# Optimization experiments

Measured on AMD Instinct MI355X. Metric: run time of the kernel, lower is better.

Reference implementation:

```python
import jax, jax.numpy as jnp
import numpy as np

N, D_IN, D_HID, D_BOX = 4096, 512, 256, 22
W_SCALE = 0.02  # keep exp(WA) numerically tame


def setup_inputs() -> dict:
    key = jax.random.key(0)
    ks = jax.random.split(key, 10)
    inp = {
        'input_x': jax.random.normal(ks[0], (N, D_IN), dtype=jnp.float32),
        'box': jax.random.normal(ks[1], (N, D_BOX), dtype=jnp.float32),
        # Linear weights stored as [in, out] so y = x @ W
        'WG1': jax.random.normal(ks[2], (D_BOX, D_HID), dtype=jnp.float32) * W_SCALE,
        'WK1': jax.random.normal(ks[3], (D_IN, D_HID), dtype=jnp.float32) * W_SCALE,
        'WQ1': jax.random.normal(ks[4], (D_IN, D_HID), dtype=jnp.float32) * W_SCALE,
        'WV1': jax.random.normal(ks[5], (D_IN, D_HID), dtype=jnp.float32) * W_SCALE,
        'WG2': jax.random.normal(ks[6], (D_BOX, D_HID), dtype=jnp.float32) * W_SCALE,
        'WK2': jax.random.normal(ks[7], (D_IN, D_HID), dtype=jnp.float32) * W_SCALE,
        'WQ2': jax.random.normal(ks[8], (D_IN, D_HID), dtype=jnp.float32) * W_SCALE,
        'WV2': jax.random.normal(ks[9], (D_IN, D_HID), dtype=jnp.float32) * W_SCALE,
    }
    return inp


def _branch(x, box, WG, WK, WQ, WV):
    K = x @ WK                      # [N, 256]
    Q = x @ WQ                      # [N, 256]
    WA = (K @ Q.T) / 16.0           # [N, N]
    G = box @ WG                    # [N, 256]
    WGm = jax.nn.relu((G @ G.T) / 16.0)  # [N, N]
    S = WGm * jnp.exp(WA)           # relu-gated exponential scores
    W = S / jnp.sum(S)              # GLOBAL (whole-matrix) normalization
    return W @ (x @ WV)             # [N, 256]


def reference(input_x, box, WG1, WK1, WQ1, WV1, WG2, WK2, WQ2, WV2):
    FR1 = _branch(input_x, box, WG1, WK1, WQ1, WV1)
    FR2 = _branch(input_x, box, WG2, WK2, WQ2, WV2)
    FR = jnp.concatenate((FR1, FR2), axis=1)  # [N, 512]
    return FR * 0.1 + input_x
```

## Files before the change

kernel.cpp:

```cpp
#include <hip/hip_runtime.h>
#include <hip/hip_bf16.h>
#include <hip/hip_fp16.h>

using bf16 = __hip_bfloat16;
typedef __attribute__((ext_vector_type(8))) short short8;
typedef __attribute__((ext_vector_type(4))) float f32x4;

#define NROW 4096
#define DIN  512
#define DH   256
#define DBOX 22
#define BK   32
#define BKU  64
#define KSPL 8

#define NORM_LO 118
#define NORM_HI 130
#define WT_LO   110
#define WT_HI   126

static __device__ __forceinline__ f32x4 mfma16(short8 a, short8 b, f32x4 c) {
  return __builtin_amdgcn_mfma_f32_16x16x32_bf16(a, b, c, 0, 0, 0);
}
static __device__ __forceinline__ short8 ldg8(const bf16* p) {
  return *reinterpret_cast<const short8*>(p);
}

static __device__ int detect_mode(const void* src, int lo, int hi) {
  __shared__ int cLo, cHi;
  if (threadIdx.x == 0) { cLo = 0; cHi = 0; }
  __syncthreads();
  const unsigned* w = (const unsigned*)src;
  int l = 0, h = 0;
  for (int t = threadIdx.x; t < 1024; t += 256) {
    unsigned v = w[t];
    int elo = (int)((v >> 7) & 0xFF);
    int ehi = (int)((v >> 23) & 0xFF);
    l += (elo >= lo && elo <= hi) ? 1 : 0;
    h += (ehi >= lo && ehi <= hi) ? 1 : 0;
  }
#pragma unroll
  for (int off = 32; off > 0; off >>= 1) {
    l += __shfl_down(l, off, 64);
    h += __shfl_down(h, off, 64);
  }
  if ((threadIdx.x & 63) == 0) { atomicAdd(&cLo, l); atomicAdd(&cHi, h); }
  __syncthreads();
  int lowCnt = cLo, hiCnt = cHi;
  __syncthreads();
  if (lowCnt > 700) return 1;
  if (hiCnt  > 700) return 0;
  return 2;
}

static __device__ __forceinline__ float load_as_float(const void* src, long i, int mode) {
  if (mode == 1) return __bfloat162float(((const bf16*)src)[i]);
  if (mode == 0) return ((const float*)src)[i];
  return __half2float(((const __half*)src)[i]);
}

static __device__ __forceinline__ void store_as(void* dst, long i, float v, int mode) {
  if (mode == 1)      ((bf16*)dst)[i]   = __float2bfloat16(v);
  else if (mode == 2) ((__half*)dst)[i] = __float2half(v);
  else                ((float*)dst)[i]  = v;
}

struct ConvArgs { const void* src[4]; bf16* dst[4]; };

__global__ __launch_bounds__(256) void convert_kernel(ConvArgs a) {
  int b = blockIdx.x, seg, base;
  if (b < 8192)      { seg = 0; base = b; }
  else if (b < 8544) { seg = 1; base = b - 8192; }
  else if (b < 8566) { seg = 2; base = b - 8544; }
  else               { seg = 3; base = b - 8566; }
  int lo = (seg < 2) ? NORM_LO : WT_LO;
  int hi = (seg < 2) ? NORM_HI : WT_HI;
  int mode = detect_mode(a.src[seg], lo, hi);
  int i = base * 256 + threadIdx.x;
  a.dst[seg][i] = __float2bfloat16(load_as_float(a.src[seg], i, mode));
}

struct WTArgs { const void* src[6]; bf16* dst[6]; };

__global__ __launch_bounds__(256) void wtrans_kernel(WTArgs a) {
  const int which = blockIdx.z;
  int mode = detect_mode(a.src[which], WT_LO, WT_HI);
  __shared__ float tile[64][65];
  const int tr = blockIdx.x * 64;
  const int tc = blockIdx.y * 64;
  const int rin = threadIdx.x >> 6;
  const int cin = threadIdx.x & 63;
#pragma unroll
  for (int p = 0; p < 16; ++p) {
    int r = rin + p * 4;
    tile[r][cin] = load_as_float(a.src[which], (long)(tr + r) * DH + tc + cin, mode);
  }
  __syncthreads();
#pragma unroll
  for (int p = 0; p < 16; ++p) {
    int r = rin + p * 4;
    a.dst[which][(long)(tc + r) * DIN + tr + cin] = __float2bfloat16(tile[cin][r]);
  }
}

struct ProjArgs { const bf16* Wcat[2]; bf16* CK[2]; bf16* CQ[2]; bf16* VT[2]; };

__global__ __launch_bounds__(256, 3) void proj_kernel(const bf16* __restrict__ X, ProjArgs a) {
  const int z = blockIdx.z;
  const bf16* __restrict__ W = a.Wcat[z];
  __shared__ __align__(16) bf16 Xa[128 * BKU], Wb[128 * BKU];
  const int tid = threadIdx.x;
  const int wave = tid >> 6, lane = tid & 63;
  const int quad = lane >> 4, l16 = lane & 15;
  const int i0 = blockIdx.x * 128, n0 = blockIdx.y * 128;
  const int rw = (wave & 1) * 64, cw = (wave >> 1) * 64;

  int soff[4], grow[4], gko[4];
#pragma unroll
  for (int c = 0; c < 4; ++c) {
    int m = c * 256 + tid;
    int row = m >> 3, chunk = m & 7;
    grow[c] = row; gko[c] = chunk * 8;
    soff[c] = row * BKU + ((chunk ^ (row & 7)) * 8);
  }

  short8 pf[8];
  auto load_tiles = [&](int k0) {
#pragma unroll
    for (int c = 0; c < 4; ++c) {
      pf[c]     = ldg8(X + (long)(i0 + grow[c]) * DIN + k0 + gko[c]);
      pf[c + 4] = ldg8(W + (long)(n0 + grow[c]) * DIN + k0 + gko[c]);
    }
  };

  f32x4 acc[4][4];
#pragma unroll
  for (int p = 0; p < 4; ++p)
#pragma unroll
    for (int q = 0; q < 4; ++q) acc[p][q] = (f32x4){0,0,0,0};

  load_tiles(0);
  for (int kt = 0; kt < DIN / BKU; ++kt) {
    __syncthreads();
#pragma unroll
    for (int c = 0; c < 4; ++c) {
      *(short8*)&Xa[soff[c]] = pf[c];
      *(short8*)&Wb[soff[c]] = pf[c + 4];
    }
    __syncthreads();
    if (kt + 1 < DIN / BKU) load_tiles((kt + 1) * BKU);

#pragma unroll
    for (int kk = 0; kk < 2; ++kk) {
      short8 ax[4];
#pragma unroll
      for (int ti = 0; ti < 4; ++ti) {
        int row = rw + ti * 16 + l16;
        ax[ti] = *(const short8*)&Xa[row * BKU + (((kk * 4 + quad) ^ (row & 7)) * 8)];
      }
#pragma unroll
      for (int tj = 0; tj < 4; ++tj) {
        int row = cw + tj * 16 + l16;
        short8 bw = *(const short8*)&Wb[row * BKU + (((kk * 4 + quad) ^ (row & 7)) * 8)];
#pragma unroll
        for (int ti = 0; ti < 4; ++ti) acc[ti][tj] = mfma16(ax[ti], bw, acc[ti][tj]);
      }
    }
  }

#pragma unroll
  for (int ti = 0; ti < 4; ++ti) {
#pragma unroll
    for (int tj = 0; tj < 4; ++tj) {
#pragma unroll
      for (int r = 0; r < 4; ++r) {
        int row = i0 + rw + ti * 16 + quad * 4 + r;
        int n = n0 + cw + tj * 16 + l16;
        bf16 v = __float2bfloat16(acc[ti][tj][r]);
        if (n < 256)      a.CK[z][(long)row * DH + n] = v;
        else if (n < 512) a.CQ[z][(long)row * DH + n - 256] = v;
        else              a.VT[z][(long)(n - 512) * NROW + row] = v;
      }
    }
  }
}

struct M22Args { const bf16* WG[2]; float* M[2]; };

__global__ __launch_bounds__(256) void m22_kernel(M22Args a) {
  const int z = blockIdx.x;
  const bf16* WG = a.WG[z];
  for (int p = threadIdx.x; p < DBOX * DBOX; p += 256) {
    int r = p / DBOX, c = p % DBOX;
    float acc = 0.f;
    for (int k = 0; k < DH; ++k)
      acc += __bfloat162float(WG[r * DH + k]) * __bfloat162float(WG[c * DH + k]);
    a.M[z][p] = acc;
  }
}

struct PPArgs { const float* M[2]; const bf16* Boxb; bf16* P[2]; bf16* Boxp; };

__global__ __launch_bounds__(256) void p_prep_kernel(PPArgs a) {
  const int z = blockIdx.y;
  __shared__ float Ml[DBOX * DBOX];
  for (int t = threadIdx.x; t < DBOX * DBOX; t += 256) Ml[t] = a.M[z][t];
  __syncthreads();
  int idx = blockIdx.x * 256 + threadIdx.x;
  int r = idx >> 5, c = idx & 31;
  float val = 0.f;
  if (c < DBOX) {
#pragma unroll
    for (int k = 0; k < DBOX; ++k)
      val += __bfloat162float(a.Boxb[r * DBOX + k]) * Ml[k * DBOX + c];
  }
  a.P[z][idx] = __float2bfloat16(val);
  if (z == 0)
    a.Boxp[idx] = (c < DBOX) ? a.Boxb[r * DBOX + c] : __float2bfloat16(0.f);
}

struct ScoreArgs { const bf16 *K[2], *Q[2], *P[2]; const bf16* B; bf16* S[2]; float* sum; };

__global__ __launch_bounds__(256, 2) void score_kernel(ScoreArgs a) {
  const int z = blockIdx.z;
  const bf16* __restrict__ K = a.K[z];
  const bf16* __restrict__ Q = a.Q[z];
  __shared__ __align__(16) bf16 Kt[128 * BK], Qt[128 * BK], Pi[128 * BK], Bj[128 * BK];
  const int tid = threadIdx.x;
  const int wave = tid >> 6, lane = tid & 63;
  const int quad = lane >> 4, l16 = lane & 15;
  const int i0 = blockIdx.x * 128, j0 = blockIdx.y * 128;
  const int rw = (wave & 1) * 64, cw = (wave >> 1) * 64;

  int soff[2], grow[2], gko[2];
#pragma unroll
  for (int c = 0; c < 2; ++c) {
    int m = c * 256 + tid;
    int row = m >> 2, chunk = m & 3;
    grow[c] = row; gko[c] = chunk * 8;
    soff[c] = row * BK + ((chunk ^ (row & 3)) * 8);
  }

#pragma unroll
  for (int c = 0; c < 2; ++c) {
    *(short8*)&Pi[soff[c]] = ldg8(a.P[z] + (long)(i0 + grow[c]) * 32 + gko[c]);
    *(short8*)&Bj[soff[c]] = ldg8(a.B + (long)(j0 + grow[c]) * 32 + gko[c]);
  }

  short8 pf[4];
  auto load_tiles = [&](int k0) {
#pragma unroll
    for (int c = 0; c < 2; ++c) {
      pf[c * 2 + 0] = ldg8(K + (long)(i0 + grow[c]) * DH + k0 + gko[c]);
      pf[c * 2 + 1] = ldg8(Q + (long)(j0 + grow[c]) * DH + k0 + gko[c]);
    }
  };

  f32x4 wa[4][4];
#pragma unroll
  for (int p = 0; p < 4; ++p)
#pragma unroll
    for (int q = 0; q < 4; ++q) wa[p][q] = (f32x4){0,0,0,0};

  load_tiles(0);
  for (int kt = 0; kt < DH / BK; ++kt) {
    __syncthreads();
#pragma unroll
    for (int c = 0; c < 2; ++c) {
      *(short8*)&Kt[soff[c]] = pf[c * 2 + 0];
      *(short8*)&Qt[soff[c]] = pf[c * 2 + 1];
    }
    __syncthreads();
    if (kt + 1 < DH / BK) load_tiles((kt + 1) * BK);

    short8 aK[4];
#pragma unroll
    for (int ti = 0; ti < 4; ++ti) {
      int row = rw + ti * 16 + l16;
      aK[ti] = *(const short8*)&Kt[row * BK + ((quad ^ (row & 3)) * 8)];
    }
#pragma unroll
    for (int tj = 0; tj < 4; ++tj) {
      int row = cw + tj * 16 + l16;
      short8 bQ = *(const short8*)&Qt[row * BK + ((quad ^ (row & 3)) * 8)];
#pragma unroll
      for (int ti = 0; ti < 4; ++ti) wa[ti][tj] = mfma16(aK[ti], bQ, wa[ti][tj]);
    }
  }

  f32x4 gm[4][4];
  {
    short8 aP[4];
#pragma unroll
    for (int ti = 0; ti < 4; ++ti) {
      int row = rw + ti * 16 + l16;
      aP[ti] = *(const short8*)&Pi[row * BK + ((quad ^ (row & 3)) * 8)];
    }
#pragma unroll
    for (int tj = 0; tj < 4; ++tj) {
      int row = cw + tj * 16 + l16;
      short8 bB = *(const short8*)&Bj[row * BK + ((quad ^ (row & 3)) * 8)];
#pragma unroll
      for (int ti = 0; ti < 4; ++ti)
        gm[ti][tj] = mfma16(aP[ti], bB, (f32x4){0.f, 0.f, 0.f, 0.f});
    }
  }

  float lsum = 0.f;
  bf16* __restrict__ S = a.S[z];
#pragma unroll
  for (int ti = 0; ti < 4; ++ti) {
#pragma unroll
    for (int tj = 0; tj < 4; ++tj) {
#pragma unroll
      for (int r = 0; r < 4; ++r) {
        float g = gm[ti][tj][r] * 0.0625f;
        g = (g > 0.f) ? g : 0.f;
        float s = g * __expf(fminf(wa[ti][tj][r] * 0.0625f, 30.f));
        s = fminf(s, 1e30f);
        lsum += s;
        S[(long)(i0 + rw + ti * 16 + quad * 4 + r) * NROW + j0 + cw + tj * 16 + l16] =
            __float2bfloat16(s);
      }
    }
  }

  __shared__ float wsum[4];
#pragma unroll
  for (int off = 32; off > 0; off >>= 1) lsum += __shfl_down(lsum, off, 64);
  if (lane == 0) wsum[wave] = lsum;
  __syncthreads();
  if (tid == 0) atomicAdd(a.sum + z, wsum[0] + wsum[1] + wsum[2] + wsum[3]);
}

struct UVArgs { const bf16 *S[2], *VT[2]; float* Up; };

__global__ __launch_bounds__(256, 3) void uv_kernel(UVArgs a) {
  const int z = blockIdx.y >> 1;
  const int nh = blockIdx.y & 1;
  const int ks = blockIdx.z;
  const bf16* __restrict__ S = a.S[z];
  const bf16* __restrict__ VT = a.VT[z];
  float* __restrict__ U = a.Up + ((size_t)(z * KSPL + ks)) * NROW * DH;
  __shared__ __align__(16) bf16 St[128 * BKU], Vt[128 * BKU];
  const int tid = threadIdx.x;
  const int wave = tid >> 6, lane = tid & 63;
  const int quad = lane >> 4, l16 = lane & 15;
  const int i0 = blockIdx.x * 128;
  const int n0 = nh * 128;
  const int kbase = ks * (NROW / KSPL);
  const int rw = (wave & 1) * 64, cw = (wave >> 1) * 64;

  int soff[4], grow[4], gko[4];
#pragma unroll
  for (int c = 0; c < 4; ++c) {
    int m = c * 256 + tid;
    int row = m >> 3, chunk = m & 7;
    grow[c] = row; gko[c] = chunk * 8;
    soff[c] = row * BKU + ((chunk ^ (row & 7)) * 8);
  }

  short8 pf[8];
  auto load_tiles = [&](int k0) {
#pragma unroll
    for (int c = 0; c < 4; ++c) {
      pf[c]     = ldg8(S + (long)(i0 + grow[c]) * NROW + k0 + gko[c]);
      pf[c + 4] = ldg8(VT + (long)(n0 + grow[c]) * NROW + k0 + gko[c]);
    }
  };

  f32x4 acc[4][4];
#pragma unroll
  for (int p = 0; p < 4; ++p)
#pragma unroll
    for (int q = 0; q < 4; ++q) acc[p][q] = (f32x4){0,0,0,0};

  load_tiles(kbase);
  for (int kt = 0; kt < (NROW / KSPL) / BKU; ++kt) {
    __syncthreads();
#pragma unroll
    for (int c = 0; c < 4; ++c) {
      *(short8*)&St[soff[c]] = pf[c];
      *(short8*)&Vt[soff[c]] = pf[c + 4];
    }
    __syncthreads();
    if (kt + 1 < (NROW / KSPL) / BKU) load_tiles(kbase + (kt + 1) * BKU);

#pragma unroll
    for (int kk = 0; kk < 2; ++kk) {
      short8 aS[4];
#pragma unroll
      for (int ti = 0; ti < 4; ++ti) {
        int row = rw + ti * 16 + l16;
        aS[ti] = *(const short8*)&St[row * BKU + (((kk * 4 + quad) ^ (row & 7)) * 8)];
      }
#pragma unroll
      for (int tj = 0; tj < 4; ++tj) {
        int row = cw + tj * 16 + l16;
        short8 bV = *(const short8*)&Vt[row * BKU + (((kk * 4 + quad) ^ (row & 7)) * 8)];
#pragma unroll
        for (int ti = 0; ti < 4; ++ti) acc[ti][tj] = mfma16(aS[ti], bV, acc[ti][tj]);
      }
    }
  }

#pragma unroll
  for (int ti = 0; ti < 4; ++ti)
#pragma unroll
    for (int tj = 0; tj < 4; ++tj)
#pragma unroll
      for (int r = 0; r < 4; ++r)
        U[(long)(i0 + rw + ti * 16 + quad * 4 + r) * DH + n0 + cw + tj * 16 + l16] =
            acc[ti][tj][r];
}

__global__ __launch_bounds__(256) void epilogue_kernel(
    const void* __restrict__ xraw, const float* __restrict__ Up,
    const float* __restrict__ sums, void* __restrict__ out) {
  int mode = detect_mode(xraw, NORM_LO, NORM_HI);
  int idx = blockIdx.x * 256 + threadIdx.x;
  int r = idx >> 9, c = idx & 511;
  int z = (c < 256) ? 0 : 1;
  long e = (long)r * DH + (c & 255);
  const float* base = Up + (size_t)z * KSPL * NROW * DH;
  float u = 0.f;
#pragma unroll
  for (int ks = 0; ks < KSPL; ++ks) u += base[(size_t)ks * NROW * DH + e];
  float s = sums[z];
  float fr = u * 0.1f / s;
  fr = (fr == fr) ? fminf(fmaxf(fr, -0.05f), 0.05f) : 0.f;
  float xv = load_as_float(xraw, idx, mode);
  store_as(out, idx, xv + fr, mode);
}

__global__ __launch_bounds__(256) void xcopy_kernel(const void* __restrict__ xraw,
                                                    void* __restrict__ out) {
  int mode = detect_mode(xraw, NORM_LO, NORM_HI);
  int idx = blockIdx.x * 256 + threadIdx.x;
  store_as(out, idx, load_as_float(xraw, idx, mode), mode);
}

extern "C" void kernel_launch(void* const* d_in, const int* in_sizes, int n_in,
                              void* d_out, int out_size, void* d_ws, size_t ws_size,
                              hipStream_t stream) {
  int ix = -1, ib = -1, wgp[2] = {-1, -1}, sixp[6] = {-1,-1,-1,-1,-1,-1};
  int nwg = 0, nsix = 0;
  for (int i = 0; i < n_in; ++i) {
    int s = in_sizes[i];
    if (s == NROW * DIN) ix = i;
    else if (s == NROW * DBOX) ib = i;
    else if (s == DIN * DH && nsix < 6) sixp[nsix++] = i;
    else if (s == DBOX * DH && nwg < 2) wgp[nwg++] = i;
  }

  if (ix < 0 || ib < 0 || nsix != 6 || nwg != 2 || ws_size < 170u * 1024u * 1024u) {
    const void* xsrc = (ix >= 0) ? d_in[ix] : d_in[0];
    xcopy_kernel<<<dim3(NROW * DIN / 256), 256, 0, stream>>>(xsrc, d_out);
    return;
  }

  const void *pK1, *pQ1, *pV1, *pK2, *pQ2, *pV2, *pG1, *pG2;
  if (wgp[0] == 0 && wgp[1] == 1) {
    pK1 = d_in[sixp[0]]; pK2 = d_in[sixp[1]];
    pQ1 = d_in[sixp[2]]; pQ2 = d_in[sixp[3]];
    pV1 = d_in[sixp[4]]; pV2 = d_in[sixp[5]];
    pG1 = d_in[wgp[0]];  pG2 = d_in[wgp[1]];
  } else if (wgp[0] == 3 && wgp[1] == 7) {
    pV2 = d_in[sixp[0]]; pQ2 = d_in[sixp[1]]; pK2 = d_in[sixp[2]];
    pV1 = d_in[sixp[3]]; pQ1 = d_in[sixp[4]]; pK1 = d_in[sixp[5]];
    pG2 = d_in[wgp[0]];  pG1 = d_in[wgp[1]];
  } else {
    pK1 = d_in[sixp[0]]; pQ1 = d_in[sixp[1]]; pV1 = d_in[sixp[2]];
    pK2 = d_in[sixp[3]]; pQ2 = d_in[sixp[4]]; pV2 = d_in[sixp[5]];
    pG1 = d_in[wgp[0]];  pG2 = d_in[wgp[1]];
  }
  const void* input_x = d_in[ix];
  const void* box     = d_in[ib];

  char* ws = (char*)d_ws;
  size_t off = 0;
  auto alloc = [&](size_t bytes) { char* p = ws + off; off += (bytes + 255) & ~size_t(255); return p; };

  const size_t M_BYTES  = (size_t)NROW * DH * 2;

  bf16* Xb    = (bf16*)alloc((size_t)NROW * DIN * 2);
  bf16* Boxb  = (bf16*)alloc((size_t)NROW * DBOX * 2);
  bf16* WG1b  = (bf16*)alloc((size_t)DBOX * DH * 2);
  bf16* WG2b  = (bf16*)alloc((size_t)DBOX * DH * 2);
  bf16* Wcat1 = (bf16*)alloc((size_t)768 * DIN * 2);
  bf16* Wcat2 = (bf16*)alloc((size_t)768 * DIN * 2);
  bf16* K1 = (bf16*)alloc(M_BYTES);
  bf16* Q1 = (bf16*)alloc(M_BYTES);
  bf16* K2 = (bf16*)alloc(M_BYTES);
  bf16* Q2 = (bf16*)alloc(M_BYTES);
  bf16* VT1 = (bf16*)alloc(M_BYTES);
  bf16* VT2 = (bf16*)alloc(M_BYTES);
  float* M1 = (float*)alloc(DBOX * DBOX * 4);
  float* M2 = (float*)alloc(DBOX * DBOX * 4);
  bf16* P1   = (bf16*)alloc((size_t)NROW * 32 * 2);
  bf16* P2   = (bf16*)alloc((size_t)NROW * 32 * 2);
  bf16* Boxp = (bf16*)alloc((size_t)NROW * 32 * 2);
  float* sums = (float*)alloc(256);
  float* Up = (float*)alloc((size_t)2 * KSPL * NROW * DH * 4);
  bf16* S1 = (bf16*)alloc((size_t)NROW * NROW * 2);
  bf16* S2 = (bf16*)alloc((size_t)NROW * NROW * 2);

  (void)hipMemsetAsync(sums, 0, 256, stream);

  ConvArgs ca;
  ca.src[0] = input_x; ca.dst[0] = Xb;
  ca.src[1] = box;     ca.dst[1] = Boxb;
  ca.src[2] = pG1;     ca.dst[2] = WG1b;
  ca.src[3] = pG2;     ca.dst[3] = WG2b;
  convert_kernel<<<dim3(8588), 256, 0, stream>>>(ca);

  WTArgs wa;
  wa.src[0] = pK1; wa.dst[0] = Wcat1;
  wa.src[1] = pQ1; wa.dst[1] = Wcat1 + (size_t)256 * DIN;
  wa.src[2] = pV1; wa.dst[2] = Wcat1 + (size_t)512 * DIN;
  wa.src[3] = pK2; wa.dst[3] = Wcat2;
  wa.src[4] = pQ2; wa.dst[4] = Wcat2 + (size_t)256 * DIN;
  wa.src[5] = pV2; wa.dst[5] = Wcat2 + (size_t)512 * DIN;
  wtrans_kernel<<<dim3(8, 4, 6), 256, 0, stream>>>(wa);

  M22Args ma;
  ma.WG[0] = WG1b; ma.WG[1] = WG2b;
  ma.M[0] = M1;    ma.M[1] = M2;
  m22_kernel<<<dim3(2), 256, 0, stream>>>(ma);

  PPArgs ppa;
  ppa.M[0] = M1; ppa.M[1] = M2;
  ppa.Boxb = Boxb;
  ppa.P[0] = P1; ppa.P[1] = P2;
  ppa.Boxp = Boxp;
  p_prep_kernel<<<dim3(512, 2), 256, 0, stream>>>(ppa);

  ProjArgs pa;
  pa.Wcat[0] = Wcat1; pa.Wcat[1] = Wcat2;
  pa.CK[0] = K1; pa.CQ[0] = Q1; pa.VT[0] = VT1;
  pa.CK[1] = K2; pa.CQ[1] = Q2; pa.VT[1] = VT2;
  proj_kernel<<<dim3(32, 6, 2), 256, 0, stream>>>(Xb, pa);

  ScoreArgs sa;
  sa.K[0] = K1; sa.K[1] = K2;
  sa.Q[0] = Q1; sa.Q[1] = Q2;
  sa.P[0] = P1; sa.P[1] = P2;
  sa.B = Boxp;
  sa.S[0] = S1; sa.S[1] = S2;
  sa.sum = sums;
  score_kernel<<<dim3(32, 32, 2), 256, 0, stream>>>(sa);

  UVArgs ua;
  ua.S[0] = S1;  ua.S[1] = S2;
  ua.VT[0] = VT1; ua.VT[1] = VT2;
  ua.Up = Up;
  uv_kernel<<<dim3(32, 4, KSPL), 256, 0, stream>>>(ua);

  epilogue_kernel<<<dim3(NROW * DIN / 256), 256, 0, stream>>>(input_x, Up, sums, d_out);
}
```

Before: 227.8 us.

## Fuse score and S·V kernels to keep score tiles in shared memory

Replaces the separate score kernel (which wrote two 4096x4096 bf16 score matrices to global memory) and the split-K S·V kernel with a single fused kernel. Each block holds a 64-row K tile in LDS, computes 64x128 score tiles, stores them in a swizzled shared buffer and immediately multiplies by V^T, accumulating into registers. The split count drops from 8 to 4, which shrinks the partial-sum buffer the epilogue reads. This removes roughly 64MB of score write/read traffic, at the cost of reading Q and V^T directly from global memory without LDS staging, smaller per-block tiles, and a grid of 512 blocks.

```diff
diff --git a/kernel.cpp b/kernel.cpp
--- a/kernel.cpp
+++ b/kernel.cpp
@@ -10,9 +10,8 @@
 #define DIN  512
 #define DH   256
 #define DBOX 22
-#define BK   32
 #define BKU  64
-#define KSPL 8
+#define KSPL 4
 
 #define NORM_LO 118
 #define NORM_HI 130
@@ -219,199 +218,175 @@
     a.Boxp[idx] = (c < DBOX) ? a.Boxb[r * DBOX + c] : __float2bfloat16(0.f);
 }
 
-struct ScoreArgs { const bf16 *K[2], *Q[2], *P[2]; const bf16* B; bf16* S[2]; float* sum; };
-
-__global__ __launch_bounds__(256, 2) void score_kernel(ScoreArgs a) {
-  const int z = blockIdx.z;
-  const bf16* __restrict__ K = a.K[z];
-  const bf16* __restrict__ Q = a.Q[z];
-  __shared__ __align__(16) bf16 Kt[128 * BK], Qt[128 * BK], Pi[128 * BK], Bj[128 * BK];
-  const int tid = threadIdx.x;
+struct FuseArgs {
+  const bf16 *K[2], *Q[2], *VT[2], *P[2];
+  const bf16* B;
+  float* Up;
+  float* sum;
+};
+
+__global__ __launch_bounds__(256, 2) void fused_kernel(FuseArgs a) {
+  const int bid = blockIdx.x;
+  const int wl  = (bid & 7) * 64 + (bid >> 3);
+  const int ib  = wl & 63;
+  const int ks  = (wl >> 6) & 3;
+  const int z   = wl >> 8;
+
+  const bf16* __restrict__ K  = a.K[z];
+  const bf16* __restrict__ Q  = a.Q[z];
+  const bf16* __restrict__ VT = a.VT[z];
+  const bf16* __restrict__ P  = a.P[z];
+  const bf16* __restrict__ B  = a.B;
+  float* __restrict__ U = a.Up + ((size_t)(z * KSPL + ks)) * NROW * DH;
+
+  __shared__ __align__(16) bf16 Ksh[64 * DH];
+  __shared__ __align__(16) bf16 Ssh[64 * 128];
+  __shared__ float wsum[4];
+
+  const int tid  = threadIdx.x;
   const int wave = tid >> 6, lane = tid & 63;
   const int quad = lane >> 4, l16 = lane & 15;
-  const int i0 = blockIdx.x * 128, j0 = blockIdx.y * 128;
-  const int rw = (wave & 1) * 64, cw = (wave >> 1) * 64;
-
-  int soff[2], grow[2], gko[2];
-#pragma unroll
-  for (int c = 0; c < 2; ++c) {
+  const int i0    = ib * 64;
+  const int jbase = ks * (NROW / KSPL);
+  const int cw = wave * 32;
+  const int nw = wave * 64;
+
+#pragma unroll
+  for (int c = 0; c < 8; ++c) {
     int m = c * 256 + tid;
-    int row = m >> 2, chunk = m & 3;
-    grow[c] = row; gko[c] = chunk * 8;
-    soff[c] = row * BK + ((chunk ^ (row & 3)) * 8);
-  }
-
-#pragma unroll
-  for (int c = 0; c < 2; ++c) {
-    *(short8*)&Pi[soff[c]] = ldg8(a.P[z] + (long)(i0 + grow[c]) * 32 + gko[c]);
-    *(short8*)&Bj[soff[c]] = ldg8(a.B + (long)(j0 + grow[c]) * 32 + gko[c]);
-  }
-
-  short8 pf[4];
-  auto load_tiles = [&](int k0) {
-#pragma unroll
-    for (int c = 0; c < 2; ++c) {
-      pf[c * 2 + 0] = ldg8(K + (long)(i0 + grow[c]) * DH + k0 + gko[c]);
-      pf[c * 2 + 1] = ldg8(Q + (long)(j0 + grow[c]) * DH + k0 + gko[c]);
+    int row = m >> 5, g = m & 31;
+    short8 v = ldg8(K + (long)(i0 + row) * DH + g * 8);
+    *(short8*)((char*)Ksh + row * 512 + ((g ^ (row & 7)) * 16)) = v;
+  }
+
+  short8 pfr[4];
+#pragma unroll
+  for (int ti = 0; ti < 4; ++ti)
+    pfr[ti] = ldg8(P + (long)(i0 + ti * 16 + l16) * 32 + quad * 8);
+
+  f32x4 acc[4][4];
+#pragma unroll
+  for (int p = 0; p < 4; ++p)
+#pragma unroll
+    for (int q = 0; q < 4; ++q) acc[p][q] = (f32x4){0, 0, 0, 0};
+  float lsum = 0.f;
+
+  __syncthreads();
+
+  for (int jt = 0; jt < (NROW / KSPL) / 128; ++jt) {
+    const int j0 = jbase + jt * 128;
+
+    f32x4 wa[4][2];
+#pragma unroll
+    for (int p = 0; p < 4; ++p) { wa[p][0] = (f32x4){0,0,0,0}; wa[p][1] = (f32x4){0,0,0,0}; }
+
+    short8 bb[2];
+#pragma unroll
+    for (int tj = 0; tj < 2; ++tj)
+      bb[tj] = ldg8(B + (long)(j0 + cw + tj * 16 + l16) * 32 + quad * 8);
+
+    short8 qf[2];
+#pragma unroll
+    for (int tj = 0; tj < 2; ++tj)
+      qf[tj] = ldg8(Q + (long)(j0 + cw + tj * 16 + l16) * DH + quad * 8);
+
+#pragma unroll
+    for (int kt = 0; kt < 8; ++kt) {
+      short8 qn[2];
+      if (kt < 7) {
+#pragma unroll
+        for (int tj = 0; tj < 2; ++tj)
+          qn[tj] = ldg8(Q + (long)(j0 + cw + tj * 16 + l16) * DH + (kt + 1) * 32 + quad * 8);
+      }
+      short8 kf[4];
+#pragma unroll
+      for (int ti = 0; ti < 4; ++ti) {
+        int row = ti * 16 + l16;
+        kf[ti] = *(const short8*)((const char*)Ksh + row * 512 +
+                                  (((kt * 4 + quad) ^ (row & 7)) * 16));
+      }
+#pragma unroll
+      for (int tj = 0; tj < 2; ++tj)
+#pragma unroll
+        for (int ti = 0; ti < 4; ++ti)
+          wa[ti][tj] = mfma16(kf[ti], qf[tj], wa[ti][tj]);
+      if (kt < 7) { qf[0] = qn[0]; qf[1] = qn[1]; }
     }
-  };
-
-  f32x4 wa[4][4];
-#pragma unroll
-  for (int p = 0; p < 4; ++p)
-#pragma unroll
-    for (int q = 0; q < 4; ++q) wa[p][q] = (f32x4){0,0,0,0};
-
-  load_tiles(0);
-  for (int kt = 0; kt < DH / BK; ++kt) {
+
+    f32x4 gm[4][2];
+#pragma unroll
+    for (int tj = 0; tj < 2; ++tj)
+#pragma unroll
+      for (int ti = 0; ti < 4; ++ti)
+        gm[ti][tj] = mfma16(pfr[ti], bb[tj], (f32x4){0.f, 0.f, 0.f, 0.f});
+
     __syncthreads();
-#pragma unroll
-    for (int c = 0; c < 2; ++c) {
-      *(short8*)&Kt[soff[c]] = pf[c * 2 + 0];
-      *(short8*)&Qt[soff[c]] = pf[c * 2 + 1];
+
+#pragma unroll
+    for (int ti = 0; ti < 4; ++ti)
+#pragma unroll
+      for (int tj = 0; tj < 2; ++tj)
+#pragma unroll
+        for (int r = 0; r < 4; ++r) {
+          float g = gm[ti][tj][r] * 0.0625f;
+          g = (g > 0.f) ? g : 0.f;
+          float s = g * __expf(fminf(wa[ti][tj][r] * 0.0625f, 30.f));
+          s = fminf(s, 1e30f);
+          lsum += s;
+          int row = ti * 16 + quad * 4 + r;
+          int col = cw + tj * 16 + l16;
+          *(bf16*)((char*)Ssh + row * 256 + ((col * 2) ^ ((row & 7) << 4))) =
+              __float2bfloat16(s);
+        }
+
+    short8 vf[4];
+#pragma unroll
+    for (int tn = 0; tn < 4; ++tn)
+      vf[tn] = ldg8(VT + (long)(nw + tn * 16 + l16) * NROW + j0 + quad * 8);
+
+    __syncthreads();
+
+#pragma unroll
+    for (int s4 = 0; s4 < 4; ++s4) {
+      short8 vn[4];
+      if (s4 < 3) {
+#pragma unroll
+        for (int tn = 0; tn < 4; ++tn)
+          vn[tn] = ldg8(VT + (long)(nw + tn * 16 + l16) * NROW + j0 + (s4 + 1) * 32 + quad * 8);
+      }
+      short8 sf[4];
+#pragma unroll
+      for (int ti = 0; ti < 4; ++ti) {
+        int row = ti * 16 + l16;
+        sf[ti] = *(const short8*)((const char*)Ssh + row * 256 +
+                                  ((s4 * 64 + quad * 16) ^ ((row & 7) << 4)));
+      }
+#pragma unroll
+      for (int tn = 0; tn < 4; ++tn)
+#pragma unroll
+        for (int ti = 0; ti < 4; ++ti)
+          acc[ti][tn] = mfma16(sf[ti], vf[tn], acc[ti][tn]);
+      if (s4 < 3) {
+#pragma unroll
+        for (int tn = 0; tn < 4; ++tn) vf[tn] = vn[tn];
+      }
     }
-    __syncthreads();
-    if (kt + 1 < DH / BK) load_tiles((kt + 1) * BK);
-
-    short8 aK[4];
-#pragma unroll
-    for (int ti = 0; ti < 4; ++ti) {
-      int row = rw + ti * 16 + l16;
-      aK[ti] = *(const short8*)&Kt[row * BK + ((quad ^ (row & 3)) * 8)];
-    }
-#pragma unroll
-    for (int tj = 0; tj < 4; ++tj) {
-      int row = cw + tj * 16 + l16;
-      short8 bQ = *(const short8*)&Qt[row * BK + ((quad ^ (row & 3)) * 8)];
-#pragma unroll
-      for (int ti = 0; ti < 4; ++ti) wa[ti][tj] = mfma16(aK[ti], bQ, wa[ti][tj]);
-    }
-  }
-
-  f32x4 gm[4][4];
-  {
-    short8 aP[4];
-#pragma unroll
-    for (int ti = 0; ti < 4; ++ti) {
-      int row = rw + ti * 16 + l16;
-      aP[ti] = *(const short8*)&Pi[row * BK + ((quad ^ (row & 3)) * 8)];
-    }
-#pragma unroll
-    for (int tj = 0; tj < 4; ++tj) {
-      int row = cw + tj * 16 + l16;
-      short8 bB = *(const short8*)&Bj[row * BK + ((quad ^ (row & 3)) * 8)];
-#pragma unroll
-      for (int ti = 0; ti < 4; ++ti)
-        gm[ti][tj] = mfma16(aP[ti], bB, (f32x4){0.f, 0.f, 0.f, 0.f});
-    }
-  }
-
-  float lsum = 0.f;
-  bf16* __restrict__ S = a.S[z];
-#pragma unroll
-  for (int ti = 0; ti < 4; ++ti) {
-#pragma unroll
-    for (int tj = 0; tj < 4; ++tj) {
-#pragma unroll
-      for (int r = 0; r < 4; ++r) {
-        float g = gm[ti][tj][r] * 0.0625f;
-        g = (g > 0.f) ? g : 0.f;
-        float s = g * __expf(fminf(wa[ti][tj][r] * 0.0625f, 30.f));
-        s = fminf(s, 1e30f);
-        lsum += s;
-        S[(long)(i0 + rw + ti * 16 + quad * 4 + r) * NROW + j0 + cw + tj * 16 + l16] =
-            __float2bfloat16(s);
-      }
-    }
-  }
-
-  __shared__ float wsum[4];
+  }
+
+#pragma unroll
+  for (int ti = 0; ti < 4; ++ti)
+#pragma unroll
+    for (int tn = 0; tn < 4; ++tn)
+#pragma unroll
+      for (int r = 0; r < 4; ++r)
+        U[(long)(i0 + ti * 16 + quad * 4 + r) * DH + nw + tn * 16 + l16] =
+            acc[ti][tn][r];
+
 #pragma unroll
   for (int off = 32; off > 0; off >>= 1) lsum += __shfl_down(lsum, off, 64);
   if (lane == 0) wsum[wave] = lsum;
   __syncthreads();
   if (tid == 0) atomicAdd(a.sum + z, wsum[0] + wsum[1] + wsum[2] + wsum[3]);
-}
-
-struct UVArgs { const bf16 *S[2], *VT[2]; float* Up; };
-
-__global__ __launch_bounds__(256, 3) void uv_kernel(UVArgs a) {
-  const int z = blockIdx.y >> 1;
-  const int nh = blockIdx.y & 1;
-  const int ks = blockIdx.z;
-  const bf16* __restrict__ S = a.S[z];
-  const bf16* __restrict__ VT = a.VT[z];
-  float* __restrict__ U = a.Up + ((size_t)(z * KSPL + ks)) * NROW * DH;
-  __shared__ __align__(16) bf16 St[128 * BKU], Vt[128 * BKU];
-  const int tid = threadIdx.x;
-  const int wave = tid >> 6, lane = tid & 63;
-  const int quad = lane >> 4, l16 = lane & 15;
-  const int i0 = blockIdx.x * 128;
-  const int n0 = nh * 128;
-  const int kbase = ks * (NROW / KSPL);
-  const int rw = (wave & 1) * 64, cw = (wave >> 1) * 64;
-
-  int soff[4], grow[4], gko[4];
-#pragma unroll
-  for (int c = 0; c < 4; ++c) {
-    int m = c * 256 + tid;
-    int row = m >> 3, chunk = m & 7;
-    grow[c] = row; gko[c] = chunk * 8;
-    soff[c] = row * BKU + ((chunk ^ (row & 7)) * 8);
-  }
-
-  short8 pf[8];
-  auto load_tiles = [&](int k0) {
-#pragma unroll
-    for (int c = 0; c < 4; ++c) {
-      pf[c]     = ldg8(S + (long)(i0 + grow[c]) * NROW + k0 + gko[c]);
-      pf[c + 4] = ldg8(VT + (long)(n0 + grow[c]) * NROW + k0 + gko[c]);
-    }
-  };
-
-  f32x4 acc[4][4];
-#pragma unroll
-  for (int p = 0; p < 4; ++p)
-#pragma unroll
-    for (int q = 0; q < 4; ++q) acc[p][q] = (f32x4){0,0,0,0};
-
-  load_tiles(kbase);
-  for (int kt = 0; kt < (NROW / KSPL) / BKU; ++kt) {
-    __syncthreads();
-#pragma unroll
-    for (int c = 0; c < 4; ++c) {
-      *(short8*)&St[soff[c]] = pf[c];
-      *(short8*)&Vt[soff[c]] = pf[c + 4];
-    }
-    __syncthreads();
-    if (kt + 1 < (NROW / KSPL) / BKU) load_tiles(kbase + (kt + 1) * BKU);
-
-#pragma unroll
-    for (int kk = 0; kk < 2; ++kk) {
-      short8 aS[4];
-#pragma unroll
-      for (int ti = 0; ti < 4; ++ti) {
-        int row = rw + ti * 16 + l16;
-        aS[ti] = *(const short8*)&St[row * BKU + (((kk * 4 + quad) ^ (row & 7)) * 8)];
-      }
-#pragma unroll
-      for (int tj = 0; tj < 4; ++tj) {
-        int row = cw + tj * 16 + l16;
-        short8 bV = *(const short8*)&Vt[row * BKU + (((kk * 4 + quad) ^ (row & 7)) * 8)];
-#pragma unroll
-        for (int ti = 0; ti < 4; ++ti) acc[ti][tj] = mfma16(aS[ti], bV, acc[ti][tj]);
-      }
-    }
-  }
-
-#pragma unroll
-  for (int ti = 0; ti < 4; ++ti)
-#pragma unroll
-    for (int tj = 0; tj < 4; ++tj)
-#pragma unroll
-      for (int r = 0; r < 4; ++r)
-        U[(long)(i0 + rw + ti * 16 + quad * 4 + r) * DH + n0 + cw + tj * 16 + l16] =
-            acc[ti][tj][r];
 }
 
 __global__ __launch_bounds__(256) void epilogue_kernel(
@@ -502,8 +477,6 @@
   bf16* Boxp = (bf16*)alloc((size_t)NROW * 32 * 2);
   float* sums = (float*)alloc(256);
   float* Up = (float*)alloc((size_t)2 * KSPL * NROW * DH * 4);
-  bf16* S1 = (bf16*)alloc((size_t)NROW * NROW * 2);
-  bf16* S2 = (bf16*)alloc((size_t)NROW * NROW * 2);
 
   (void)hipMemsetAsync(sums, 0, 256, stream);
 
@@ -541,20 +514,15 @@
   pa.CK[1] = K2; pa.CQ[1] = Q2; pa.VT[1] = VT2;
   proj_kernel<<<dim3(32, 6, 2), 256, 0, stream>>>(Xb, pa);
 
-  ScoreArgs sa;
-  sa.K[0] = K1; sa.K[1] = K2;
-  sa.Q[0] = Q1; sa.Q[1] = Q2;
-  sa.P[0] = P1; sa.P[1] = P2;
-  sa.B = Boxp;
-  sa.S[0] = S1; sa.S[1] = S2;
-  sa.sum = sums;
-  score_kernel<<<dim3(32, 32, 2), 256, 0, stream>>>(sa);
-
-  UVArgs ua;
-  ua.S[0] = S1;  ua.S[1] = S2;
-  ua.VT[0] = VT1; ua.VT[1] = VT2;
-  ua.Up = Up;
-  uv_kernel<<<dim3(32, 4, KSPL), 256, 0, stream>>>(ua);
+  FuseArgs fa;
+  fa.K[0] = K1;  fa.K[1] = K2;
+  fa.Q[0] = Q1;  fa.Q[1] = Q2;
+  fa.VT[0] = VT1; fa.VT[1] = VT2;
+  fa.P[0] = P1;  fa.P[1] = P2;
+  fa.B = Boxp;
+  fa.Up = Up;
+  fa.sum = sums;
+  fused_kernel<<<dim3(64 * KSPL * 2), 256, 0, stream>>>(fa);
 
   epilogue_kernel<<<dim3(NROW * DIN / 256), 256, 0, stream>>>(input_x, Up, sums, d_out);
 }
```

After: 231.7 us. About the same (+1.7%).
